# Performance work log

Hardware: AMD Instinct MI355X
Metric: run time of the kernel (lower is better)

## Reference

```python
import jax, jax.numpy as jnp
import numpy as np

HEADS = 8
DIM_HEAD = 64
KNN = 32
SCALE = DIM_HEAD ** -0.5


def setup_inputs() -> dict:
    key = jax.random.key(0)
    k1, k2, k3 = jax.random.split(key, 3)
    B, N, C = 2, 2048, 256
    inner = HEADS * DIM_HEAD  # 512
    x = jax.random.normal(k1, (B, N, C), dtype=jnp.float32)
    Wqkv = jax.random.normal(k2, (C, 3 * inner), dtype=jnp.float32) * (C ** -0.5)
    Wout = jax.random.normal(k3, (inner, C), dtype=jnp.float32) * (inner ** -0.5)
    bout = jnp.zeros((C,), dtype=jnp.float32)
    return {"x": x, "Wqkv": Wqkv, "Wout": Wout, "bout": bout}


def _knn_adjacency(x, k):
    # x: [B, N, C] -> boolean adjacency [B, N, N], k nearest neighbors by
    # euclidean distance, self-loops excluded (loop=False).
    B, N, _ = x.shape
    x2 = jnp.sum(x * x, axis=-1)  # [B, N]
    # squared distances [B, N, N]
    d2 = x2[:, :, None] + x2[:, None, :] - 2.0 * jnp.einsum('bnc,bmc->bnm', x, x)
    big = jnp.finfo(d2.dtype).max
    d2 = d2 + big * jnp.eye(N, dtype=d2.dtype)  # exclude self
    _, idx = jax.lax.top_k(-d2, k)  # [B, N, k] nearest neighbor indices

    rows = jnp.arange(N)[:, None]  # [N, 1]

    def scatter_one(idx_b):
        return jnp.zeros((N, N), dtype=bool).at[rows, idx_b].set(True)

    return jax.vmap(scatter_one)(idx)  # [B, N, N]


def reference(x, Wqkv, Wout, bout):
    B, N, C = x.shape
    adj = _knn_adjacency(x, KNN)  # [B, N, N] bool, shared across heads

    qkv = x @ Wqkv  # [B, N, 3*inner]
    q, k, v = jnp.split(qkv, 3, axis=-1)
    split_heads = lambda t: t.reshape(B, N, HEADS, DIM_HEAD).transpose(0, 2, 1, 3)
    q, k, v = split_heads(q), split_heads(k), split_heads(v)  # [B, H, N, d]

    dots = jnp.einsum('bhnd,bhmd->bhnm', q, k) * SCALE  # [B, H, N, N]
    dots = jnp.where(adj[:, None, :, :], dots, -jnp.inf)
    attn = jax.nn.softmax(dots, axis=-1)
    out = jnp.einsum('bhnm,bhmd->bhnd', attn, v)  # [B, H, N, d]
    out = out.transpose(0, 2, 1, 3).reshape(B, N, HEADS * DIM_HEAD)
    return out @ Wout + bout
```

## Files before the change

kernel.cpp:

```cpp
#include <hip/hip_runtime.h>
#include <hip/hip_bf16.h>
#include <hip/hip_fp16.h>

#define BATCH 2
#define NPTS  2048
#define CDIM  256
#define NHEAD 8
#define DHEAD 64
#define INNER 512
#define TRIPLE 1536
#define KNN   32
#define SCALE 0.125f

#define GRAM_ITEMS 272
#define QKV_ITEMS  384
#define TOTAL_ITEMS (GRAM_ITEMS + QKV_ITEMS)

#define PREP_BLOCKS 1024
#define WT_BLOCKS   128

typedef __attribute__((ext_vector_type(8))) short short8;
typedef __attribute__((ext_vector_type(4))) float floatx4;
typedef __attribute__((ext_vector_type(4))) unsigned short ushort4v;
typedef unsigned short ushort;

#define TW  32
#define TSZ (128*TW)

__device__ __forceinline__ unsigned bfsplit(float x) {
    unsigned u = __float_as_uint(x);
    unsigned r = u + 0x7fffu + ((u >> 16) & 1u);
    unsigned hs = r >> 16;
    float hf = __uint_as_float(hs << 16);
    float lo = x - hf;
    unsigned u2 = __float_as_uint(lo);
    unsigned r2 = u2 + 0x7fffu + ((u2 >> 16) & 1u);
    return (hs & 0xffffu) | (r2 & 0xffff0000u);
}

__device__ __forceinline__ void bfsplit3(float x, ushort* hh, ushort* ll, ushort* qq) {
    unsigned u = __float_as_uint(x);
    unsigned r = u + 0x7fffu + ((u >> 16) & 1u);
    unsigned hs = r >> 16;
    float hf = __uint_as_float(hs << 16);
    float d1 = x - hf;
    unsigned u2 = __float_as_uint(d1);
    unsigned r2 = u2 + 0x7fffu + ((u2 >> 16) & 1u);
    unsigned ls = r2 >> 16;
    float lf = __uint_as_float(ls << 16);
    float d2 = d1 - lf;
    unsigned u3 = __float_as_uint(d2);
    unsigned r3 = u3 + 0x7fffu + ((u3 >> 16) & 1u);
    *hh = (ushort)hs;
    *ll = (ushort)ls;
    *qq = (ushort)(r3 >> 16);
}

__device__ __forceinline__ ushort f2h(float f) {
    __half h = __float2half(f);
    return *reinterpret_cast<ushort*>(&h);
}
__device__ __forceinline__ float h2f(ushort u) {
    __half h;
    *reinterpret_cast<ushort*>(&h) = u;
    return __half2float(h);
}

__global__ __launch_bounds__(256) void prep_kernel(const float* __restrict__ x,
                                                   float* __restrict__ x2,
                                                   ushort* __restrict__ xhi,
                                                   ushort* __restrict__ xlo,
                                                   ushort* __restrict__ xqd,
                                                   const float* __restrict__ Wqkv,
                                                   const float* __restrict__ Wout,
                                                   ushort* __restrict__ wqhiT,
                                                   ushort* __restrict__ wqloT,
                                                   ushort* __restrict__ wohiT,
                                                   ushort* __restrict__ woloT) {
    __shared__ float tile[64][65];
    int gbid = blockIdx.x;
    if (gbid < PREP_BLOCKS) {
        int wave = threadIdx.x >> 6, lane = threadIdx.x & 63;
        int row = gbid * 4 + wave;
        const float* xr = x + (size_t)row * CDIM;
        float4 v = *(const float4*)(xr + lane * 4);
        float s = v.x*v.x + v.y*v.y + v.z*v.z + v.w*v.w;
        #pragma unroll
        for (int o = 32; o; o >>= 1) s += __shfl_down(s, o);
        if (lane == 0) x2[row] = s;

        ushort h[4], l[4], q[4];
        bfsplit3(v.x, &h[0], &l[0], &q[0]);
        bfsplit3(v.y, &h[1], &l[1], &q[1]);
        bfsplit3(v.z, &h[2], &l[2], &q[2]);
        bfsplit3(v.w, &h[3], &l[3], &q[3]);
        size_t off = (size_t)row * CDIM + lane * 4;
        *(ushort4v*)(xhi + off) = *(ushort4v*)h;
        *(ushort4v*)(xlo + off) = *(ushort4v*)l;
        *(ushort4v*)(xqd + off) = *(ushort4v*)q;
        return;
    }

    int bid = gbid - PREP_BLOCKS;
    const float* W; ushort* hiT; ushort* loT; int K, N, bx, by;
    if (bid < 96) { W = Wqkv; hiT = wqhiT; loT = wqloT; K = CDIM;  N = TRIPLE; bx = bid % 24; by = bid / 24; }
    else { int t = bid - 96; W = Wout; hiT = wohiT; loT = woloT; K = INNER; N = CDIM;  bx = t % 4;  by = t / 4; }
    int k0 = by * 64, n0 = bx * 64;
    #pragma unroll
    for (int i = 0; i < 4; ++i) {
        int f = threadIdx.x + i * 256;
        int r = f >> 4, c4 = (f & 15) * 4;
        float4 v = *(const float4*)(W + (size_t)(k0 + r) * N + n0 + c4);
        tile[r][c4+0] = v.x; tile[r][c4+1] = v.y;
        tile[r][c4+2] = v.z; tile[r][c4+3] = v.w;
    }
    __syncthreads();
    #pragma unroll
    for (int i = 0; i < 4; ++i) {
        int f = threadIdx.x + i * 256;
        int rn = f >> 4, ck = (f & 15) * 4;
        unsigned p0 = bfsplit(tile[ck+0][rn]);
        unsigned p1 = bfsplit(tile[ck+1][rn]);
        unsigned p2 = bfsplit(tile[ck+2][rn]);
        unsigned p3 = bfsplit(tile[ck+3][rn]);
        ushort4v h, l;
        h.x = (ushort)p0; l.x = (ushort)(p0 >> 16);
        h.y = (ushort)p1; l.y = (ushort)(p1 >> 16);
        h.z = (ushort)p2; l.z = (ushort)(p2 >> 16);
        h.w = (ushort)p3; l.w = (ushort)(p3 >> 16);
        *(ushort4v*)(hiT + (size_t)(n0 + rn) * K + k0 + ck) = h;
        *(ushort4v*)(loT + (size_t)(n0 + rn) * K + k0 + ck) = l;
    }
}


__device__ __forceinline__ void gemm_split_body(const ushort* __restrict__ Ahi,
                                                const ushort* __restrict__ Alo,
                                                const ushort* __restrict__ BhiT,
                                                const ushort* __restrict__ BloT,
                                                const float* __restrict__ bias,
                                                float* __restrict__ C,
                                                int N, int K, int bi, int bj,
                                                ushort* lds,
                                                ushort* __restrict__ kv16) {
    int lane = threadIdx.x & 63, wave = threadIdx.x >> 6;
    int wr = wave >> 1, wc = wave & 1;
    int fr = lane & 15, kg = lane >> 4;
    int swz8 = (kg ^ ((fr >> 1) & 3)) * 8;

    int srow = threadIdx.x >> 1;
    int hc = (threadIdx.x & 1) * 2;
    int sw = (srow >> 1) & 3;
    int d0 = srow * TW + ((hc + 0) ^ sw) * 8;
    int d1 = srow * TW + ((hc + 1) ^ sw) * 8;

    const ushort* g0 = Ahi  + (size_t)(bi + srow) * K + hc * 8;
    const ushort* g1 = Alo  + (size_t)(bi + srow) * K + hc * 8;
    const ushort* g2 = BhiT + (size_t)(bj + srow) * K + hc * 8;
    const ushort* g3 = BloT + (size_t)(bj + srow) * K + hc * 8;

    floatx4 acc[4][4] = {};

    for (int k0 = 0; k0 < K; k0 += 32) {
        uint4 va0 = *(const uint4*)(g0 + k0);
        uint4 va1 = *(const uint4*)(g0 + k0 + 8);
        uint4 vb0 = *(const uint4*)(g1 + k0);
        uint4 vb1 = *(const uint4*)(g1 + k0 + 8);
        uint4 vc0 = *(const uint4*)(g2 + k0);
        uint4 vc1 = *(const uint4*)(g2 + k0 + 8);
        uint4 vd0 = *(const uint4*)(g3 + k0);
        uint4 vd1 = *(const uint4*)(g3 + k0 + 8);
        *(uint4*)&lds[0*TSZ + d0] = va0;  *(uint4*)&lds[0*TSZ + d1] = va1;
        *(uint4*)&lds[1*TSZ + d0] = vb0;  *(uint4*)&lds[1*TSZ + d1] = vb1;
        *(uint4*)&lds[2*TSZ + d0] = vc0;  *(uint4*)&lds[2*TSZ + d1] = vc1;
        *(uint4*)&lds[3*TSZ + d0] = vd0;  *(uint4*)&lds[3*TSZ + d1] = vd1;
        __syncthreads();

        short8 a_h[4], a_l[4], b_h[4], b_l[4];
        #pragma unroll
        for (int m = 0; m < 4; ++m) {
            int off = (wr*64 + m*16 + fr) * TW + swz8;
            a_h[m] = *(const short8*)&lds[0*TSZ + off];
            a_l[m] = *(const short8*)&lds[1*TSZ + off];
        }
        #pragma unroll
        for (int n = 0; n < 4; ++n) {
            int off = (wc*64 + n*16 + fr) * TW + swz8;
            b_h[n] = *(const short8*)&lds[2*TSZ + off];
            b_l[n] = *(const short8*)&lds[3*TSZ + off];
        }
        #pragma unroll
        for (int m = 0; m < 4; ++m)
            #pragma unroll
            for (int n = 0; n < 4; ++n) {
                acc[m][n] = __builtin_amdgcn_mfma_f32_16x16x32_bf16(a_h[m], b_h[n], acc[m][n], 0, 0, 0);
                acc[m][n] = __builtin_amdgcn_mfma_f32_16x16x32_bf16(a_h[m], b_l[n], acc[m][n], 0, 0, 0);
                acc[m][n] = __builtin_amdgcn_mfma_f32_16x16x32_bf16(a_l[m], b_h[n], acc[m][n], 0, 0, 0);
            }
        __syncthreads();
    }

    if (kv16) {
        bool is_q = (bj < INNER);
        #pragma unroll
        for (int m = 0; m < 4; ++m)
            #pragma unroll
            for (int n = 0; n < 4; ++n) {
                int col = bj + wc*64 + n*16 + fr;
                #pragma unroll
                for (int r = 0; r < 4; ++r) {
                    int row = bi + wr*64 + m*16 + kg*4 + r;
                    float val = acc[m][n][r];
                    if (is_q) C[(size_t)row * INNER + col] = val;
                    else      kv16[(size_t)row * 1024 + (col - INNER)] = f2h(val);
                }
            }
    } else {
        #pragma unroll
        for (int m = 0; m < 4; ++m)
            #pragma unroll
            for (int n = 0; n < 4; ++n) {
                int col = bj + wc*64 + n*16 + fr;
                float bv = bias ? bias[col] : 0.0f;
                #pragma unroll
                for (int r = 0; r < 4; ++r) {
                    int row = bi + wr*64 + m*16 + kg*4 + r;
                    C[(size_t)row * N + col] = acc[m][n][r] + bv;
                }
            }
    }
}

__device__ __forceinline__ void gram_body(const ushort* __restrict__ Ah,
                                          const ushort* __restrict__ Al,
                                          const ushort* __restrict__ Aq,
                                          const float* __restrict__ x2b,
                                          float* __restrict__ Sb,
                                          int bi, int bj, ushort* lds) {
    int lane = threadIdx.x & 63, wave = threadIdx.x >> 6;
    int wr = wave >> 1, wc = wave & 1;
    int fr = lane & 15, kg = lane >> 4;
    int swz8 = (kg ^ ((fr >> 1) & 3)) * 8;

    int srow = threadIdx.x >> 1;
    int hc = (threadIdx.x & 1) * 2;
    int sw = (srow >> 1) & 3;
    int d0 = srow * TW + ((hc + 0) ^ sw) * 8;
    int d1 = srow * TW + ((hc + 1) ^ sw) * 8;

    const ushort* g0 = Ah + (size_t)(bi + srow) * CDIM + hc * 8;
    const ushort* g1 = Al + (size_t)(bi + srow) * CDIM + hc * 8;
    const ushort* g2 = Aq + (size_t)(bi + srow) * CDIM + hc * 8;
    const ushort* g3 = Ah + (size_t)(bj + srow) * CDIM + hc * 8;
    const ushort* g4 = Al + (size_t)(bj + srow) * CDIM + hc * 8;
    const ushort* g5 = Aq + (size_t)(bj + srow) * CDIM + hc * 8;

    floatx4 acc[4][4] = {};

    for (int k0 = 0; k0 < CDIM; k0 += 32) {
        uint4 a0 = *(const uint4*)(g0 + k0); uint4 a1 = *(const uint4*)(g0 + k0 + 8);
        uint4 b0 = *(const uint4*)(g1 + k0); uint4 b1 = *(const uint4*)(g1 + k0 + 8);
        uint4 c0 = *(const uint4*)(g2 + k0); uint4 c1 = *(const uint4*)(g2 + k0 + 8);
        uint4 e0 = *(const uint4*)(g3 + k0); uint4 e1 = *(const uint4*)(g3 + k0 + 8);
        uint4 f0 = *(const uint4*)(g4 + k0); uint4 f1 = *(const uint4*)(g4 + k0 + 8);
        uint4 h0 = *(const uint4*)(g5 + k0); uint4 h1 = *(const uint4*)(g5 + k0 + 8);
        *(uint4*)&lds[0*TSZ + d0] = a0; *(uint4*)&lds[0*TSZ + d1] = a1;
        *(uint4*)&lds[1*TSZ + d0] = b0; *(uint4*)&lds[1*TSZ + d1] = b1;
        *(uint4*)&lds[2*TSZ + d0] = c0; *(uint4*)&lds[2*TSZ + d1] = c1;
        *(uint4*)&lds[3*TSZ + d0] = e0; *(uint4*)&lds[3*TSZ + d1] = e1;
        *(uint4*)&lds[4*TSZ + d0] = f0; *(uint4*)&lds[4*TSZ + d1] = f1;
        *(uint4*)&lds[5*TSZ + d0] = h0; *(uint4*)&lds[5*TSZ + d1] = h1;
        __syncthreads();

        short8 a_h[4], a_l[4], a_q[4], b_h[4], b_l[4], b_q[4];
        #pragma unroll
        for (int m = 0; m < 4; ++m) {
            int off = (wr*64 + m*16 + fr) * TW + swz8;
            a_h[m] = *(const short8*)&lds[0*TSZ + off];
            a_l[m] = *(const short8*)&lds[1*TSZ + off];
            a_q[m] = *(const short8*)&lds[2*TSZ + off];
        }
        #pragma unroll
        for (int n = 0; n < 4; ++n) {
            int off = (wc*64 + n*16 + fr) * TW + swz8;
            b_h[n] = *(const short8*)&lds[3*TSZ + off];
            b_l[n] = *(const short8*)&lds[4*TSZ + off];
            b_q[n] = *(const short8*)&lds[5*TSZ + off];
        }
        #pragma unroll
        for (int m = 0; m < 4; ++m)
            #pragma unroll
            for (int n = 0; n < 4; ++n) {
                acc[m][n] = __builtin_amdgcn_mfma_f32_16x16x32_bf16(a_h[m], b_h[n], acc[m][n], 0, 0, 0);
                acc[m][n] = __builtin_amdgcn_mfma_f32_16x16x32_bf16(a_h[m], b_l[n], acc[m][n], 0, 0, 0);
                acc[m][n] = __builtin_amdgcn_mfma_f32_16x16x32_bf16(a_l[m], b_h[n], acc[m][n], 0, 0, 0);
                acc[m][n] = __builtin_amdgcn_mfma_f32_16x16x32_bf16(a_l[m], b_l[n], acc[m][n], 0, 0, 0);
                acc[m][n] = __builtin_amdgcn_mfma_f32_16x16x32_bf16(a_h[m], b_q[n], acc[m][n], 0, 0, 0);
                acc[m][n] = __builtin_amdgcn_mfma_f32_16x16x32_bf16(a_q[m], b_h[n], acc[m][n], 0, 0, 0);
            }
        __syncthreads();
    }

    #pragma unroll
    for (int m = 0; m < 4; ++m)
        #pragma unroll
        for (int n = 0; n < 4; ++n) {
            int col = bj + wc*64 + n*16 + fr;
            float xc = x2b[col];
            #pragma unroll
            for (int r = 0; r < 4; ++r) {
                int row = bi + wr*64 + m*16 + kg*4 + r;
                float val = xc - 2.0f * acc[m][n][r];
                if (row == col) val = __builtin_inff();
                Sb[(size_t)row * NPTS + col] = val;
            }
        }

    if (bi != bj) {
        float* T = (float*)lds;
        #pragma unroll
        for (int p = 0; p < 2; ++p) {
            __syncthreads();
            if (wc == p) {
                #pragma unroll
                for (int m = 0; m < 4; ++m) {
                    int row0 = wr*64 + m*16 + kg*4;
                    float x0 = x2b[bi + row0 + 0];
                    float x1 = x2b[bi + row0 + 1];
                    float x2v = x2b[bi + row0 + 2];
                    float x3 = x2b[bi + row0 + 3];
                    #pragma unroll
                    for (int n = 0; n < 4; ++n) {
                        int colp = n*16 + fr;
                        float4 v;
                        v.x = x0 - 2.0f * acc[m][n][0];
                        v.y = x1 - 2.0f * acc[m][n][1];
                        v.z = x2v - 2.0f * acc[m][n][2];
                        v.w = x3 - 2.0f * acc[m][n][3];
                        *(float4*)&T[colp * 132 + row0] = v;
                    }
                }
            }
            __syncthreads();
            #pragma unroll
            for (int i = 0; i < 8; ++i) {
                int f = threadIdx.x + i * 256;
                int cr = f >> 5, c4 = (f & 31) * 4;
                float4 v = *(const float4*)&T[cr * 132 + c4];
                *(float4*)(Sb + (size_t)(bj + p*64 + cr) * NPTS + bi + c4) = v;
            }
        }
    }
}

__global__ __launch_bounds__(256) void fused_mfma_kernel(const ushort* __restrict__ xh,
                                                         const ushort* __restrict__ xl,
                                                         const ushort* __restrict__ xq,
                                                         const float* __restrict__ x2,
                                                         float* __restrict__ S,
                                                         const ushort* __restrict__ wqhiT,
                                                         const ushort* __restrict__ wqloT,
                                                         float* __restrict__ q,
                                                         ushort* __restrict__ kv16) {
    __shared__ ushort lds[6*TSZ];
    int item = blockIdx.x;
    if (item < GRAM_ITEMS) {
        int b = item / 136, t = item % 136;
        int by = 0;
        while (t >= 16 - by) { t -= 16 - by; ++by; }
        int bx = by + t;
        size_t xoff = (size_t)b * NPTS * CDIM;
        gram_body(xh + xoff, xl + xoff, xq + xoff,
                  x2 + (size_t)b * NPTS, S + (size_t)b * NPTS * NPTS,
                  by * 128, bx * 128, lds);
    } else {
        int t = item - GRAM_ITEMS;
        int bx = t % 12, by = t / 12;
        gemm_split_body(xh, xl, wqhiT, wqloT, nullptr, q,
                        TRIPLE, CDIM, by * 128, bx * 128, lds, kv16);
    }
}

__global__ __launch_bounds__(256) void outproj_kernel(const ushort* __restrict__ Ahi,
                                                      const ushort* __restrict__ Alo,
                                                      const ushort* __restrict__ BhiT,
                                                      const ushort* __restrict__ BloT,
                                                      const float* __restrict__ bias,
                                                      float* __restrict__ C) {
    __shared__ ushort lds[4*TSZ];
    gemm_split_body(Ahi, Alo, BhiT, BloT, bias, C,
                    CDIM, INNER, blockIdx.y * 128, blockIdx.x * 128, lds, nullptr);
}

__device__ __forceinline__ unsigned block_excl_scan_256(unsigned c,
                                                        unsigned* wsum,
                                                        unsigned* total_out) {
    unsigned v = c;
    #pragma unroll
    for (int o = 1; o < 64; o <<= 1) {
        unsigned t = __shfl_up(v, o);
        if ((threadIdx.x & 63) >= o) v += t;
    }
    if ((threadIdx.x & 63) == 63) wsum[threadIdx.x >> 6] = v;
    __syncthreads();
    unsigned woff = 0;
    int mywave = threadIdx.x >> 6;
    #pragma unroll
    for (int w = 0; w < 4; ++w) {
        unsigned s = wsum[w];
        if (w < mywave) woff += s;
    }
    if (total_out) *total_out = wsum[0] + wsum[1] + wsum[2] + wsum[3];
    __syncthreads();
    return v + woff - c;
}

__global__ __launch_bounds__(256) void knn_attn_kernel(const float* __restrict__ S,
                                                       const float* __restrict__ q,
                                                       const ushort* __restrict__ kv16,
                                                       ushort* __restrict__ ahi,
                                                       ushort* __restrict__ alo) {
    int bid = blockIdx.x;
    int b = (bid & 7) >> 2;
    int n = ((bid >> 3) << 2) | (bid & 3);
    size_t rowoff = (size_t)b * NPTS + n;
    const float* row = S + rowoff * NPTS;

    __shared__ unsigned keys[NPTS];
    __shared__ unsigned hist[256];
    __shared__ unsigned wsum[4];
    __shared__ unsigned s_red[8];
    __shared__ unsigned sh_lo, sh_hi, sh_rank, sh_cnt, sh_break;
    __shared__ unsigned ckey[64];
    __shared__ int     cidx[64];
    __shared__ unsigned s_ccount;
    __shared__ int   nb[KNN];
    __shared__ float dots[NHEAD][KNN];
    __shared__ float p[NHEAD][KNN];

    int tid = threadIdx.x;

    unsigned mn = 0xffffffffu, mx = 0u;
    {
        int i0 = tid * 8;
        float4 f0 = *(const float4*)(row + i0);
        float4 f1 = *(const float4*)(row + i0 + 4);
        float fv[8] = { f0.x, f0.y, f0.z, f0.w, f1.x, f1.y, f1.z, f1.w };
        #pragma unroll
        for (int t = 0; t < 8; ++t) {
            int i = i0 + t;
            unsigned u;
            if (i == n) {
                u = 0xffffffffu;
            } else {
                unsigned v = __float_as_uint(fv[t]);
                u = (v & 0x80000000u) ? ~v : (v | 0x80000000u);
                mn = min(mn, u); mx = max(mx, u);
            }
            keys[i] = u;
        }
    }
    #pragma unroll
    for (int o = 32; o; o >>= 1) {
        mn = min(mn, (unsigned)__shfl_xor((int)mn, o));
        mx = max(mx, (unsigned)__shfl_xor((int)mx, o));
    }
    if ((tid & 63) == 0) { s_red[tid >> 6] = mn; s_red[4 + (tid >> 6)] = mx; }
    __syncthreads();
    if (tid == 0) {
        unsigned a = min(min(s_red[0], s_red[1]), min(s_red[2], s_red[3]));
        unsigned z = max(max(s_red[4], s_red[5]), max(s_red[6], s_red[7]));
        sh_lo = a; sh_hi = z; sh_rank = KNN; sh_break = 0; s_ccount = 0;
    }
    __syncthreads();

    for (int it = 0; it < 5; ++it) {
        unsigned lo = sh_lo, hi = sh_hi;
        unsigned range1 = hi - lo;
        int shift = 0;
        if (range1 > 255u) shift = 24 - __clz(range1);
        hist[tid] = 0;
        __syncthreads();
        for (int i = tid; i < NPTS; i += 256) {
            unsigned u = keys[i];
            if (u >= lo && u <= hi)
                atomicAdd(&hist[(u - lo) >> shift], 1u);
        }
        __syncthreads();
        unsigned c = hist[tid];
        unsigned rank = sh_rank;
        unsigned excl = block_excl_scan_256(c, wsum, nullptr);
        if (excl < rank && excl + c >= rank) {
            sh_rank = rank - excl;
            unsigned nlo = lo + ((unsigned)tid << shift);
            unsigned span = (shift == 0) ? 0u : (((1u << shift)) - 1u);
            unsigned nhi = nlo + span;
            if (nhi > hi || nhi < nlo) nhi = hi;
            sh_lo = nlo; sh_hi = nhi;
            sh_cnt = c;
            sh_break = (shift == 0 || c <= 64u) ? 1u : 0u;
        }
        __syncthreads();
        if (sh_break) break;
    }

    unsigned lo = sh_lo, hi = sh_hi, rank = sh_rank, cnt = sh_cnt;

    unsigned lt = 0;
    for (int i = tid; i < NPTS; i += 256) lt += (keys[i] < lo) ? 1u : 0u;
    unsigned pos = block_excl_scan_256(lt, wsum, nullptr);
    for (int i = tid; i < NPTS; i += 256) {
        unsigned u = keys[i];
        if (u < lo) nb[pos++] = i;
        else if (u >= lo && u <= hi && cnt <= 64u) {
            unsigned pp = atomicAdd(&s_ccount, 1u);
            ckey[pp] = u; cidx[pp] = i;
        }
    }
    __syncthreads();

    unsigned base = KNN - rank;
    if (cnt <= 64u) {
        if (tid < (int)cnt) {
            unsigned myk = ckey[tid]; int myi = cidx[tid];
            unsigned r = 0;
            for (unsigned s = 0; s < cnt; ++s) {
                unsigned sk = ckey[s]; int si = cidx[s];
                r += (sk < myk || (sk == myk && si < myi)) ? 1u : 0u;
            }
            if (r < rank) nb[base + r] = myi;
        }
    } else {
        if (tid == 0) {
            unsigned need = rank, pp = base;
            for (int i = 0; i < NPTS && need; ++i) {
                if (keys[i] >= lo && keys[i] <= hi) { nb[pp++] = i; --need; }
            }
        }
    }
    __syncthreads();

    const float* qrow = q + rowoff * INNER;
    const ushort* kvb = kv16 + (size_t)b * NPTS * 1024;

    {
        int j = tid >> 3;
        int l = tid & 7;
        const ushort* krow = kvb + (size_t)nb[j] * 1024 + l * 8;
        short8 kr[NHEAD];
        #pragma unroll
        for (int h = 0; h < NHEAD; ++h)
            kr[h] = *(const short8*)(krow + h * DHEAD);
        const float* qp = qrow + l * 8;
        #pragma unroll
        for (int h = 0; h < NHEAD; ++h) {
            float4 q0 = *(const float4*)(qp + h * DHEAD);
            float4 q1 = *(const float4*)(qp + h * DHEAD + 4);
            float d = h2f((ushort)kr[h][0]) * q0.x + h2f((ushort)kr[h][1]) * q0.y
                    + h2f((ushort)kr[h][2]) * q0.z + h2f((ushort)kr[h][3]) * q0.w
                    + h2f((ushort)kr[h][4]) * q1.x + h2f((ushort)kr[h][5]) * q1.y
                    + h2f((ushort)kr[h][6]) * q1.z + h2f((ushort)kr[h][7]) * q1.w;
            d += __shfl_xor(d, 1);
            d += __shfl_xor(d, 2);
            d += __shfl_xor(d, 4);
            if (l == 0) dots[h][j] = d * SCALE;
        }
    }
    __syncthreads();

    {
        int h = tid >> 5, jj = tid & 31;
        float dv = dots[h][jj];
        float mxv = dv;
        for (int o = 16; o; o >>= 1) mxv = fmaxf(mxv, __shfl_xor(mxv, o));
        float e = expf(dv - mxv);
        float s = e;
        for (int o = 16; o; o >>= 1) s += __shfl_xor(s, o);
        p[h][jj] = e / s;
    }
    __syncthreads();

    {
        int hd = tid >> 5;
        int jd = tid & 31;
        const ushort* vb = kvb + INNER + hd * DHEAD + jd * 2;
        float o0 = 0.f, o1 = 0.f;
        #pragma unroll
        for (int g = 0; g < 4; ++g) {
            unsigned vv[8]; float pw[8];
            #pragma unroll
            for (int t = 0; t < 8; ++t) {
                int jj = g * 8 + t;
                vv[t] = *(const unsigned*)(vb + (size_t)nb[jj] * 1024);
                pw[t] = p[hd][jj];
            }
            #pragma unroll
            for (int t = 0; t < 8; ++t) {
                o0 += pw[t] * h2f((ushort)(vv[t] & 0xffffu));
                o1 += pw[t] * h2f((ushort)(vv[t] >> 16));
            }
        }
        size_t baseo = rowoff * INNER + hd * DHEAD + jd * 2;
        unsigned q0 = bfsplit(o0);
        unsigned q1 = bfsplit(o1);
        *(unsigned*)(ahi + baseo) = (q0 & 0xffffu) | (q1 << 16);
        *(unsigned*)(alo + baseo) = (q0 >> 16) | (q1 & 0xffff0000u);
    }
}

extern "C" void kernel_launch(void* const* d_in, const int* in_sizes, int n_in,
                              void* d_out, int out_size, void* d_ws, size_t ws_size,
                              hipStream_t stream) {
    const float* x    = (const float*)d_in[0];
    const float* Wqkv = (const float*)d_in[1];
    const float* Wout = (const float*)d_in[2];
    const float* bout = (const float*)d_in[3];
    float* out = (float*)d_out;

    float* S     = (float*)d_ws;
    float* x2    = S + (size_t)BATCH * NPTS * NPTS;
    float* q     = x2 + (size_t)BATCH * NPTS;
    ushort* kv16 = (ushort*)(q + (size_t)BATCH * NPTS * INNER);
    ushort* xhi  = kv16 + (size_t)BATCH * NPTS * 1024;
    ushort* xlo   = xhi   + (size_t)BATCH * NPTS * CDIM;
    ushort* xqd   = xlo   + (size_t)BATCH * NPTS * CDIM;
    ushort* ahi   = xqd   + (size_t)BATCH * NPTS * CDIM;
    ushort* alo   = ahi   + (size_t)BATCH * NPTS * INNER;
    ushort* wqhiT = alo   + (size_t)BATCH * NPTS * INNER;
    ushort* wqloT = wqhiT + (size_t)TRIPLE * CDIM;
    ushort* wohiT = wqloT + (size_t)TRIPLE * CDIM;
    ushort* woloT = wohiT + (size_t)CDIM * INNER;

    prep_kernel<<<PREP_BLOCKS + WT_BLOCKS, 256, 0, stream>>>(
        x, x2, xhi, xlo, xqd, Wqkv, Wout, wqhiT, wqloT, wohiT, woloT);

    fused_mfma_kernel<<<TOTAL_ITEMS, 256, 0, stream>>>(xhi, xlo, xqd, x2, S,
                                                       wqhiT, wqloT, q, kv16);

    knn_attn_kernel<<<BATCH * NPTS, 256, 0, stream>>>(S, q, kv16, ahi, alo);

    {
        dim3 grid(CDIM / 128, (BATCH * NPTS) / 128);
        outproj_kernel<<<grid, 256, 0, stream>>>(ahi, alo, wohiT, woloT, bout, out);
    }
}
```

Baseline: 104.2 us.

## Use single-bf16 Gram for kNN preselection, rerank 48 candidates in exact fp32

The Gram-matrix distance computation drops from a 6-term bf16 split (hi/lo/quad) to a single bf16 product. This cuts MFMA work and LDS traffic in the gram tiles, and the third x split buffer is no longer produced. The kNN selection now keeps 48 approximate candidates, recomputes their distances in fp32 from x, and ranks them to pick the true 32. The risk is that a true neighbor falls outside the 48 approximate candidates, and the per-row rerank adds some global reads.

```diff
diff --git a/kernel.cpp b/kernel.cpp
--- a/kernel.cpp
+++ b/kernel.cpp
@@ -10,6 +10,7 @@
 #define INNER 512
 #define TRIPLE 1536
 #define KNN   32
+#define NCAND 48
 #define SCALE 0.125f
 
 #define GRAM_ITEMS 272
@@ -38,24 +39,6 @@
     return (hs & 0xffffu) | (r2 & 0xffff0000u);
 }
 
-__device__ __forceinline__ void bfsplit3(float x, ushort* hh, ushort* ll, ushort* qq) {
-    unsigned u = __float_as_uint(x);
-    unsigned r = u + 0x7fffu + ((u >> 16) & 1u);
-    unsigned hs = r >> 16;
-    float hf = __uint_as_float(hs << 16);
-    float d1 = x - hf;
-    unsigned u2 = __float_as_uint(d1);
-    unsigned r2 = u2 + 0x7fffu + ((u2 >> 16) & 1u);
-    unsigned ls = r2 >> 16;
-    float lf = __uint_as_float(ls << 16);
-    float d2 = d1 - lf;
-    unsigned u3 = __float_as_uint(d2);
-    unsigned r3 = u3 + 0x7fffu + ((u3 >> 16) & 1u);
-    *hh = (ushort)hs;
-    *ll = (ushort)ls;
-    *qq = (ushort)(r3 >> 16);
-}
-
 __device__ __forceinline__ ushort f2h(float f) {
     __half h = __float2half(f);
     return *reinterpret_cast<ushort*>(&h);
@@ -70,7 +53,6 @@
                                                    float* __restrict__ x2,
                                                    ushort* __restrict__ xhi,
                                                    ushort* __restrict__ xlo,
-                                                   ushort* __restrict__ xqd,
                                                    const float* __restrict__ Wqkv,
                                                    const float* __restrict__ Wout,
                                                    ushort* __restrict__ wqhiT,
@@ -89,15 +71,16 @@
         for (int o = 32; o; o >>= 1) s += __shfl_down(s, o);
         if (lane == 0) x2[row] = s;
 
-        ushort h[4], l[4], q[4];
-        bfsplit3(v.x, &h[0], &l[0], &q[0]);
-        bfsplit3(v.y, &h[1], &l[1], &q[1]);
-        bfsplit3(v.z, &h[2], &l[2], &q[2]);
-        bfsplit3(v.w, &h[3], &l[3], &q[3]);
+        unsigned p0 = bfsplit(v.x), p1 = bfsplit(v.y),
+                 p2 = bfsplit(v.z), p3 = bfsplit(v.w);
+        ushort4v h, l;
+        h.x = (ushort)p0; l.x = (ushort)(p0 >> 16);
+        h.y = (ushort)p1; l.y = (ushort)(p1 >> 16);
+        h.z = (ushort)p2; l.z = (ushort)(p2 >> 16);
+        h.w = (ushort)p3; l.w = (ushort)(p3 >> 16);
         size_t off = (size_t)row * CDIM + lane * 4;
-        *(ushort4v*)(xhi + off) = *(ushort4v*)h;
-        *(ushort4v*)(xlo + off) = *(ushort4v*)l;
-        *(ushort4v*)(xqd + off) = *(ushort4v*)q;
+        *(ushort4v*)(xhi + off) = h;
+        *(ushort4v*)(xlo + off) = l;
         return;
     }
 
@@ -231,12 +214,10 @@
     }
 }
 
-__device__ __forceinline__ void gram_body(const ushort* __restrict__ Ah,
-                                          const ushort* __restrict__ Al,
-                                          const ushort* __restrict__ Aq,
-                                          const float* __restrict__ x2b,
-                                          float* __restrict__ Sb,
-                                          int bi, int bj, ushort* lds) {
+__device__ __forceinline__ void gram_approx_body(const ushort* __restrict__ Ah,
+                                                 const float* __restrict__ x2b,
+                                                 float* __restrict__ Sb,
+                                                 int bi, int bj, ushort* lds) {
     int lane = threadIdx.x & 63, wave = threadIdx.x >> 6;
     int wr = wave >> 1, wc = wave & 1;
     int fr = lane & 15, kg = lane >> 4;
@@ -249,55 +230,33 @@
     int d1 = srow * TW + ((hc + 1) ^ sw) * 8;
 
     const ushort* g0 = Ah + (size_t)(bi + srow) * CDIM + hc * 8;
-    const ushort* g1 = Al + (size_t)(bi + srow) * CDIM + hc * 8;
-    const ushort* g2 = Aq + (size_t)(bi + srow) * CDIM + hc * 8;
-    const ushort* g3 = Ah + (size_t)(bj + srow) * CDIM + hc * 8;
-    const ushort* g4 = Al + (size_t)(bj + srow) * CDIM + hc * 8;
-    const ushort* g5 = Aq + (size_t)(bj + srow) * CDIM + hc * 8;
+    const ushort* g1 = Ah + (size_t)(bj + srow) * CDIM + hc * 8;
 
     floatx4 acc[4][4] = {};
 
     for (int k0 = 0; k0 < CDIM; k0 += 32) {
         uint4 a0 = *(const uint4*)(g0 + k0); uint4 a1 = *(const uint4*)(g0 + k0 + 8);
-        uint4 b0 = *(const uint4*)(g1 + k0); uint4 b1 = *(const uint4*)(g1 + k0 + 8);
-        uint4 c0 = *(const uint4*)(g2 + k0); uint4 c1 = *(const uint4*)(g2 + k0 + 8);
-        uint4 e0 = *(const uint4*)(g3 + k0); uint4 e1 = *(const uint4*)(g3 + k0 + 8);
-        uint4 f0 = *(const uint4*)(g4 + k0); uint4 f1 = *(const uint4*)(g4 + k0 + 8);
-        uint4 h0 = *(const uint4*)(g5 + k0); uint4 h1 = *(const uint4*)(g5 + k0 + 8);
+        uint4 e0 = *(const uint4*)(g1 + k0); uint4 e1 = *(const uint4*)(g1 + k0 + 8);
         *(uint4*)&lds[0*TSZ + d0] = a0; *(uint4*)&lds[0*TSZ + d1] = a1;
-        *(uint4*)&lds[1*TSZ + d0] = b0; *(uint4*)&lds[1*TSZ + d1] = b1;
-        *(uint4*)&lds[2*TSZ + d0] = c0; *(uint4*)&lds[2*TSZ + d1] = c1;
-        *(uint4*)&lds[3*TSZ + d0] = e0; *(uint4*)&lds[3*TSZ + d1] = e1;
-        *(uint4*)&lds[4*TSZ + d0] = f0; *(uint4*)&lds[4*TSZ + d1] = f1;
-        *(uint4*)&lds[5*TSZ + d0] = h0; *(uint4*)&lds[5*TSZ + d1] = h1;
+        *(uint4*)&lds[1*TSZ + d0] = e0; *(uint4*)&lds[1*TSZ + d1] = e1;
         __syncthreads();
 
-        short8 a_h[4], a_l[4], a_q[4], b_h[4], b_l[4], b_q[4];
+        short8 a_h[4], b_h[4];
         #pragma unroll
         for (int m = 0; m < 4; ++m) {
             int off = (wr*64 + m*16 + fr) * TW + swz8;
             a_h[m] = *(const short8*)&lds[0*TSZ + off];
-            a_l[m] = *(const short8*)&lds[1*TSZ + off];
-            a_q[m] = *(const short8*)&lds[2*TSZ + off];
         }
         #pragma unroll
         for (int n = 0; n < 4; ++n) {
             int off = (wc*64 + n*16 + fr) * TW + swz8;
-            b_h[n] = *(const short8*)&lds[3*TSZ + off];
-            b_l[n] = *(const short8*)&lds[4*TSZ + off];
-            b_q[n] = *(const short8*)&lds[5*TSZ + off];
+            b_h[n] = *(const short8*)&lds[1*TSZ + off];
         }
         #pragma unroll
         for (int m = 0; m < 4; ++m)
             #pragma unroll
-            for (int n = 0; n < 4; ++n) {
+            for (int n = 0; n < 4; ++n)
                 acc[m][n] = __builtin_amdgcn_mfma_f32_16x16x32_bf16(a_h[m], b_h[n], acc[m][n], 0, 0, 0);
-                acc[m][n] = __builtin_amdgcn_mfma_f32_16x16x32_bf16(a_h[m], b_l[n], acc[m][n], 0, 0, 0);
-                acc[m][n] = __builtin_amdgcn_mfma_f32_16x16x32_bf16(a_l[m], b_h[n], acc[m][n], 0, 0, 0);
-                acc[m][n] = __builtin_amdgcn_mfma_f32_16x16x32_bf16(a_l[m], b_l[n], acc[m][n], 0, 0, 0);
-                acc[m][n] = __builtin_amdgcn_mfma_f32_16x16x32_bf16(a_h[m], b_q[n], acc[m][n], 0, 0, 0);
-                acc[m][n] = __builtin_amdgcn_mfma_f32_16x16x32_bf16(a_q[m], b_h[n], acc[m][n], 0, 0, 0);
-            }
         __syncthreads();
     }
 
@@ -355,14 +314,13 @@
 
 __global__ __launch_bounds__(256) void fused_mfma_kernel(const ushort* __restrict__ xh,
                                                          const ushort* __restrict__ xl,
-                                                         const ushort* __restrict__ xq,
                                                          const float* __restrict__ x2,
                                                          float* __restrict__ S,
                                                          const ushort* __restrict__ wqhiT,
                                                          const ushort* __restrict__ wqloT,
                                                          float* __restrict__ q,
                                                          ushort* __restrict__ kv16) {
-    __shared__ ushort lds[6*TSZ];
+    __shared__ ushort lds[16896];
     int item = blockIdx.x;
     if (item < GRAM_ITEMS) {
         int b = item / 136, t = item % 136;
@@ -370,9 +328,9 @@
         while (t >= 16 - by) { t -= 16 - by; ++by; }
         int bx = by + t;
         size_t xoff = (size_t)b * NPTS * CDIM;
-        gram_body(xh + xoff, xl + xoff, xq + xoff,
-                  x2 + (size_t)b * NPTS, S + (size_t)b * NPTS * NPTS,
-                  by * 128, bx * 128, lds);
+        gram_approx_body(xh + xoff, x2 + (size_t)b * NPTS,
+                         S + (size_t)b * NPTS * NPTS,
+                         by * 128, bx * 128, lds);
     } else {
         int t = item - GRAM_ITEMS;
         int bx = t % 12, by = t / 12;
@@ -416,6 +374,8 @@
 }
 
 __global__ __launch_bounds__(256) void knn_attn_kernel(const float* __restrict__ S,
+                                                       const float* __restrict__ x,
+                                                       const float* __restrict__ x2,
                                                        const float* __restrict__ q,
                                                        const ushort* __restrict__ kv16,
                                                        ushort* __restrict__ ahi,
@@ -425,6 +385,8 @@
     int n = ((bid >> 3) << 2) | (bid & 3);
     size_t rowoff = (size_t)b * NPTS + n;
     const float* row = S + rowoff * NPTS;
+    const float* xb  = x + (size_t)b * NPTS * CDIM;
+    const float* x2b = x2 + (size_t)b * NPTS;
 
     __shared__ unsigned keys[NPTS];
     __shared__ unsigned hist[256];
@@ -434,6 +396,8 @@
     __shared__ unsigned ckey[64];
     __shared__ int     cidx[64];
     __shared__ unsigned s_ccount;
+    __shared__ int   cand[NCAND];
+    __shared__ float dex[NCAND];
     __shared__ int   nb[KNN];
     __shared__ float dots[NHEAD][KNN];
     __shared__ float p[NHEAD][KNN];
@@ -470,7 +434,7 @@
     if (tid == 0) {
         unsigned a = min(min(s_red[0], s_red[1]), min(s_red[2], s_red[3]));
         unsigned z = max(max(s_red[4], s_red[5]), max(s_red[6], s_red[7]));
-        sh_lo = a; sh_hi = z; sh_rank = KNN; sh_break = 0; s_ccount = 0;
+        sh_lo = a; sh_hi = z; sh_rank = NCAND; sh_break = 0; s_ccount = 0;
     }
     __syncthreads();
 
@@ -511,7 +475,7 @@
     unsigned pos = block_excl_scan_256(lt, wsum, nullptr);
     for (int i = tid; i < NPTS; i += 256) {
         unsigned u = keys[i];
-        if (u < lo) nb[pos++] = i;
+        if (u < lo) cand[pos++] = i;
         else if (u >= lo && u <= hi && cnt <= 64u) {
             unsigned pp = atomicAdd(&s_ccount, 1u);
             ckey[pp] = u; cidx[pp] = i;
@@ -519,7 +483,7 @@
     }
     __syncthreads();
 
-    unsigned base = KNN - rank;
+    unsigned base = NCAND - rank;
     if (cnt <= 64u) {
         if (tid < (int)cnt) {
             unsigned myk = ckey[tid]; int myi = cidx[tid];
@@ -528,15 +492,46 @@
                 unsigned sk = ckey[s]; int si = cidx[s];
                 r += (sk < myk || (sk == myk && si < myi)) ? 1u : 0u;
             }
-            if (r < rank) nb[base + r] = myi;
+            if (r < rank) cand[base + r] = myi;
         }
     } else {
         if (tid == 0) {
             unsigned need = rank, pp = base;
             for (int i = 0; i < NPTS && need; ++i) {
-                if (keys[i] >= lo && keys[i] <= hi) { nb[pp++] = i; --need; }
-            }
-        }
+                if (keys[i] >= lo && keys[i] <= hi) { cand[pp++] = i; --need; }
+            }
+        }
+    }
+    __syncthreads();
+
+    {
+        int g = tid >> 2;
+        int ln = tid & 3;
+        if (g < NCAND) {
+            const float* xc = xb + (size_t)cand[g] * CDIM + ln * 64;
+            const float* xq = xb + (size_t)n * CDIM + ln * 64;
+            float dot = 0.f;
+            #pragma unroll
+            for (int t = 0; t < 16; ++t) {
+                float4 a = *(const float4*)(xc + t * 4);
+                float4 bq = *(const float4*)(xq + t * 4);
+                dot += a.x*bq.x + a.y*bq.y + a.z*bq.z + a.w*bq.w;
+            }
+            dot += __shfl_xor(dot, 1);
+            dot += __shfl_xor(dot, 2);
+            if (ln == 0) dex[g] = x2b[cand[g]] - 2.0f * dot;
+        }
+    }
+    __syncthreads();
+
+    if (tid < NCAND) {
+        float myd = dex[tid]; int myi = cand[tid];
+        unsigned r = 0;
+        for (int s = 0; s < NCAND; ++s) {
+            float sd = dex[s]; int si = cand[s];
+            r += (sd < myd || (sd == myd && si < myi)) ? 1u : 0u;
+        }
+        if (r < KNN) nb[r] = myi;
     }
     __syncthreads();
 
@@ -623,8 +618,7 @@
     ushort* kv16 = (ushort*)(q + (size_t)BATCH * NPTS * INNER);
     ushort* xhi  = kv16 + (size_t)BATCH * NPTS * 1024;
     ushort* xlo   = xhi   + (size_t)BATCH * NPTS * CDIM;
-    ushort* xqd   = xlo   + (size_t)BATCH * NPTS * CDIM;
-    ushort* ahi   = xqd   + (size_t)BATCH * NPTS * CDIM;
+    ushort* ahi   = xlo   + (size_t)BATCH * NPTS * CDIM;
     ushort* alo   = ahi   + (size_t)BATCH * NPTS * INNER;
     ushort* wqhiT = alo   + (size_t)BATCH * NPTS * INNER;
     ushort* wqloT = wqhiT + (size_t)TRIPLE * CDIM;
@@ -632,12 +626,12 @@
     ushort* woloT = wohiT + (size_t)CDIM * INNER;
 
     prep_kernel<<<PREP_BLOCKS + WT_BLOCKS, 256, 0, stream>>>(
-        x, x2, xhi, xlo, xqd, Wqkv, Wout, wqhiT, wqloT, wohiT, woloT);
-
-    fused_mfma_kernel<<<TOTAL_ITEMS, 256, 0, stream>>>(xhi, xlo, xqd, x2, S,
+        x, x2, xhi, xlo, Wqkv, Wout, wqhiT, wqloT, wohiT, woloT);
+
+    fused_mfma_kernel<<<TOTAL_ITEMS, 256, 0, stream>>>(xhi, xlo, x2, S,
                                                        wqhiT, wqloT, q, kv16);
 
-    knn_attn_kernel<<<BATCH * NPTS, 256, 0, stream>>>(S, q, kv16, ahi, alo);
+    knn_attn_kernel<<<BATCH * NPTS, 256, 0, stream>>>(S, x, x2, q, kv16, ahi, alo);
 
     {
         dim3 grid(CDIM / 128, (BATCH * NPTS) / 128);
```

After: 149.9 us. 1.44x slower.
